# Optimization experiments

Measured on AMD Instinct MI355X. Metric: run time of the kernel, lower is better.

The kernel has to match this reference:

```python
import jax, jax.numpy as jnp
import numpy as np

EPS = 1e-8


def setup_inputs() -> dict:
    key = jax.random.key(0)
    k1, k2, k3 = jax.random.split(key, 3)
    N, M, D = 200000, 64, 128
    X = jax.random.normal(k1, (N, D), dtype=jnp.float32)
    r = jax.random.uniform(k2, (N, M), dtype=jnp.float32)
    mus = jax.random.normal(k3, (M, D), dtype=jnp.float32)
    return {"X": X, "r": r, "mus": mus}


def _pairwise_l2_sim(X, mus):
    # sim = -||x - mu||_2, computed via the Gram trick to avoid an [N,M,D] intermediate
    x2 = jnp.sum(X * X, axis=-1, keepdims=True)          # [N,1]
    m2 = jnp.sum(mus * mus, axis=-1)[None, :]            # [1,M]
    sq = x2 + m2 - 2.0 * (X @ mus.T)                     # [N,M]
    return -jnp.sqrt(jnp.maximum(sq, 0.0))


def reference(X, r, mus):
    N = X.shape[0]
    sim = _pairwise_l2_sim(X, mus)                       # [N,M]
    sim_z = -jnp.log(jax.nn.sigmoid(sim) + EPS)          # [N,M]
    loss = jnp.sum(r * sim_z) / N
    return loss
```

## Files before the change

### kernel.cpp

```cpp
#include <hip/hip_runtime.h>
#include <math.h>

#define D_DIM 128
#define M_CLUSTERS 64
#define ROWS 64
#define BLOCK 256
#define RBLOCK 256

typedef __bf16 bf16x8 __attribute__((ext_vector_type(8)));
typedef float f32x4 __attribute__((ext_vector_type(4)));

union B8 {
    int4 i;
    bf16x8 b;
};

__device__ __forceinline__ float zval(float sq) {
    float dd = sqrtf(fmaxf(sq, 0.0f));
    float sg = __fdividef(1.0f, 1.0f + __expf(dd));
    return -__logf(sg + 1e-8f);
}

__device__ __forceinline__ void gload16(const void* g, void* l) {
    __builtin_amdgcn_global_load_lds(
        (const __attribute__((address_space(1))) unsigned int*)g,
        (__attribute__((address_space(3))) unsigned int*)l, 16, 0, 0);
}

__global__ void iso_prep(const float4* __restrict__ mus4, int4* __restrict__ muB4,
                         float* __restrict__ m2) {
    const int f = blockIdx.x * 256 + threadIdx.x;
    float4 v0 = mus4[f * 2 + 0];
    float4 v1 = mus4[f * 2 + 1];
    B8 p;
    p.b[0] = (__bf16)v0.x; p.b[1] = (__bf16)v0.y;
    p.b[2] = (__bf16)v0.z; p.b[3] = (__bf16)v0.w;
    p.b[4] = (__bf16)v1.x; p.b[5] = (__bf16)v1.y;
    p.b[6] = (__bf16)v1.z; p.b[7] = (__bf16)v1.w;
    muB4[f] = p.i;
    if (blockIdx.x == 0 && threadIdx.x < M_CLUSTERS) {
        const float4* mv = mus4 + threadIdx.x * (D_DIM / 4);
        float s = 0.f;
#pragma unroll
        for (int d = 0; d < D_DIM / 4; ++d) {
            float4 v = mv[d];
            s = fmaf(v.x, v.x, s);
            s = fmaf(v.y, v.y, s);
            s = fmaf(v.z, v.z, s);
            s = fmaf(v.w, v.w, s);
        }
        m2[threadIdx.x] = s;
    }
}

__global__ __launch_bounds__(BLOCK, 4) void iso_main(
        const float* __restrict__ X, const float* __restrict__ r,
        const int4* __restrict__ muB4, const float* __restrict__ m2g,
        float* __restrict__ partials, int N) {
    __shared__ __align__(16) char lds_raw[ROWS * 512 + M_CLUSTERS * 256];
    __shared__ float pl[BLOCK];

    const int tid = threadIdx.x;
    const int lane = tid & 63;
    const int la = lane & 15;
    const int lg = lane >> 4;
    const int w = tid >> 6;
    const int rowbase = blockIdx.x * ROWS;

    char* xs = lds_raw;
    char* bs = lds_raw + ROWS * 512;

#pragma unroll
    for (int c = 0; c < 8; ++c) {
        int rr = c * 2 + (lane >> 5);
        int grow = rowbase + w * 16 + rr;
        grow = grow < N ? grow : N - 1;
        int slot = (lane & 31) ^ (rr & 7);
        gload16(X + (size_t)grow * D_DIM + slot * 4,
                xs + (size_t)w * 8192 + c * 1024);
    }
#pragma unroll
    for (int i = 0; i < 4; ++i) {
        int k = w * 4 + i;
        int c = k * 4 + (lane >> 4);
        int slot = (lane & 15) ^ (c & 7);
        gload16(muB4 + c * 16 + slot, bs + k * 1024);
    }

    float rv[4][4];
    const int erow = rowbase + w * 16 + lg * 4;
#pragma unroll
    for (int q = 0; q < 4; ++q) {
        int rrow = erow + q;
        const float* rr_ = r + (size_t)(rrow < N ? rrow : N - 1) * M_CLUSTERS + la;
#pragma unroll
        for (int cb = 0; cb < 4; ++cb)
            rv[q][cb] = (rrow < N) ? rr_[cb * 16] : 0.f;
    }
    float m2r[4];
#pragma unroll
    for (int cb = 0; cb < 4; ++cb) m2r[cb] = m2g[cb * 16 + la];

    asm volatile("s_waitcnt vmcnt(0)" ::: "memory");
    __syncthreads();

    f32x4 acc[4];
#pragma unroll
    for (int cb = 0; cb < 4; ++cb)
#pragma unroll
        for (int q = 0; q < 4; ++q) acc[cb][q] = 0.f;
    float x2 = 0.f;

    const char* xw = xs + (size_t)w * 8192;
#pragma unroll
    for (int kk = 0; kk < 4; ++kk) {
        int s0 = kk * 8 + lg * 2;
        float4 xa = *(const float4*)(xw + la * 512 + ((s0) ^ (la & 7)) * 16);
        float4 xb = *(const float4*)(xw + la * 512 + ((s0 + 1) ^ (la & 7)) * 16);
        B8 a;
        a.b[0] = (__bf16)xa.x; a.b[1] = (__bf16)xa.y;
        a.b[2] = (__bf16)xa.z; a.b[3] = (__bf16)xa.w;
        a.b[4] = (__bf16)xb.x; a.b[5] = (__bf16)xb.y;
        a.b[6] = (__bf16)xb.z; a.b[7] = (__bf16)xb.w;
        x2 = fmaf(xa.x, xa.x, x2); x2 = fmaf(xa.y, xa.y, x2);
        x2 = fmaf(xa.z, xa.z, x2); x2 = fmaf(xa.w, xa.w, x2);
        x2 = fmaf(xb.x, xb.x, x2); x2 = fmaf(xb.y, xb.y, x2);
        x2 = fmaf(xb.z, xb.z, x2); x2 = fmaf(xb.w, xb.w, x2);
        B8 b[4];
#pragma unroll
        for (int cb = 0; cb < 4; ++cb) {
            int cc = cb * 16 + la;
            int t = (kk * 4 + lg) ^ (cc & 7);
            b[cb].i = *(const int4*)(bs + cc * 256 + t * 16);
        }
#pragma unroll
        for (int cb = 0; cb < 4; ++cb)
            acc[cb] = __builtin_amdgcn_mfma_f32_16x16x32_bf16(a.b, b[cb].b,
                                                              acc[cb], 0, 0, 0);
    }

    x2 += __shfl_xor(x2, 16, 64);
    x2 += __shfl_xor(x2, 32, 64);
    float x2r[4];
#pragma unroll
    for (int q = 0; q < 4; ++q) x2r[q] = __shfl(x2, lg * 4 + q, 64);

    float partial = 0.f;
#pragma unroll
    for (int q = 0; q < 4; ++q)
#pragma unroll
        for (int cb = 0; cb < 4; ++cb) {
            float sq = x2r[q] + m2r[cb] - 2.0f * acc[cb][q];
            partial = fmaf(rv[q][cb], zval(sq), partial);
        }

    pl[tid] = partial;
    __syncthreads();
    if (tid < 64) {
        float s = pl[lane] + pl[64 + lane] + pl[128 + lane] + pl[192 + lane];
#pragma unroll
        for (int off = 32; off > 0; off >>= 1)
            s += __shfl_down(s, off, 64);
        if (lane == 0) partials[blockIdx.x] = s;
    }
}

__global__ void iso_reduce(const float* __restrict__ partials, int nblocks,
                           float* __restrict__ out, float invN) {
    float s = 0.f;
    for (int i = threadIdx.x; i < nblocks; i += RBLOCK) s += partials[i];
#pragma unroll
    for (int off = 32; off > 0; off >>= 1)
        s += __shfl_down(s, off, 64);
    __shared__ float wsum[RBLOCK / 64];
    const int lane = threadIdx.x & 63;
    const int wid = threadIdx.x >> 6;
    if (lane == 0) wsum[wid] = s;
    __syncthreads();
    if (threadIdx.x == 0)
        out[0] = (wsum[0] + wsum[1] + wsum[2] + wsum[3]) * invN;
}

extern "C" void kernel_launch(void* const* d_in, const int* in_sizes, int n_in,
                              void* d_out, int out_size, void* d_ws, size_t ws_size,
                              hipStream_t stream) {
    const float* X = (const float*)d_in[0];
    const float* r = (const float*)d_in[1];
    const float* mus = (const float*)d_in[2];
    const int N = in_sizes[0] / D_DIM;

    int4* muB4 = (int4*)d_ws;
    float* m2 = (float*)((char*)d_ws + 16384);
    float* partials = m2 + M_CLUSTERS;

    const int nblocks = (N + ROWS - 1) / ROWS;

    hipLaunchKernelGGL(iso_prep, dim3(4), dim3(256), 0, stream,
                       (const float4*)mus, muB4, m2);
    hipLaunchKernelGGL(iso_main, dim3(nblocks), dim3(BLOCK), 0, stream,
                       X, r, muB4, m2, partials, N);
    hipLaunchKernelGGL(iso_reduce, dim3(1), dim3(RBLOCK), 0, stream,
                       partials, nblocks, (float*)d_out, 1.0f / (float)N);
}
```

Before: 42.76 us.

## Process four row tiles per block and prefetch next X tile during epilogue

Each block now loops over four 64-row tiles instead of one, so the block count drops by four. The bf16 mu matrix and m2 are loaded into LDS once per block. After each tile's MFMA phase, the next tile's X rows are issued asynchronously into the same LDS buffer, so the load overlaps the sqrt/exp/log epilogue and the loads of r. The goal is to hide global-load latency and amortise setup. In exchange there is less block-level parallelism, a single X buffer, and one wasted prefetch past the last tile. The __syncthreads before the vmcnt wait may not guarantee that the mu LDS copies issued by other waves are visible.

New measurement: 48.12 us. 1.13x slower.

```diff
diff --git a/kernel.cpp b/kernel.cpp
--- a/kernel.cpp
+++ b/kernel.cpp
@@ -3,7 +3,8 @@
 
 #define D_DIM 128
 #define M_CLUSTERS 64
-#define ROWS 64
+#define TILE_ROWS 64
+#define TPB 4
 #define BLOCK 256
 #define RBLOCK 256
 
@@ -57,7 +58,8 @@
         const float* __restrict__ X, const float* __restrict__ r,
         const int4* __restrict__ muB4, const float* __restrict__ m2g,
         float* __restrict__ partials, int N) {
-    __shared__ __align__(16) char lds_raw[ROWS * 512 + M_CLUSTERS * 256];
+    __shared__ __align__(16) char xs_raw[4 * 8192];
+    __shared__ __align__(16) char bs_raw[16384];
     __shared__ float pl[BLOCK];
 
     const int tid = threadIdx.x;
@@ -65,20 +67,13 @@
     const int la = lane & 15;
     const int lg = lane >> 4;
     const int w = tid >> 6;
-    const int rowbase = blockIdx.x * ROWS;
-
-    char* xs = lds_raw;
-    char* bs = lds_raw + ROWS * 512;
-
-#pragma unroll
-    for (int c = 0; c < 8; ++c) {
-        int rr = c * 2 + (lane >> 5);
-        int grow = rowbase + w * 16 + rr;
-        grow = grow < N ? grow : N - 1;
-        int slot = (lane & 31) ^ (rr & 7);
-        gload16(X + (size_t)grow * D_DIM + slot * 4,
-                xs + (size_t)w * 8192 + c * 1024);
-    }
+
+    char* xw = xs_raw + w * 8192;
+    char* bs = bs_raw;
+
+    const int rr = (lane >> 5);
+    const int xslot = (lane & 31);
+
 #pragma unroll
     for (int i = 0; i < 4; ++i) {
         int k = w * 4 + i;
@@ -86,73 +81,104 @@
         int slot = (lane & 15) ^ (c & 7);
         gload16(muB4 + c * 16 + slot, bs + k * 1024);
     }
-
-    float rv[4][4];
-    const int erow = rowbase + w * 16 + lg * 4;
-#pragma unroll
-    for (int q = 0; q < 4; ++q) {
-        int rrow = erow + q;
-        const float* rr_ = r + (size_t)(rrow < N ? rrow : N - 1) * M_CLUSTERS + la;
+    {
+        int rowbase = blockIdx.x * (TPB * TILE_ROWS) + w * 16;
+#pragma unroll
+        for (int c = 0; c < 8; ++c) {
+            int row = c * 2 + rr;
+            int grow = rowbase + row;
+            grow = grow < N ? grow : N - 1;
+            int slot = xslot ^ (row & 7);
+            gload16(X + (size_t)grow * D_DIM + slot * 4, xw + c * 1024);
+        }
+    }
+    float m2r[4];
+#pragma unroll
+    for (int cb = 0; cb < 4; ++cb) m2r[cb] = m2g[cb * 16 + la];
+    __syncthreads();
+
+    float partial = 0.f;
+
+    for (int t = 0; t < TPB; ++t) {
+        const int rowbase = (blockIdx.x * TPB + t) * TILE_ROWS + w * 16;
+
+        float rv[4][4];
+        const int erow = rowbase + lg * 4;
+#pragma unroll
+        for (int q = 0; q < 4; ++q) {
+            int rrow = erow + q;
+            const float* rr_ =
+                r + (size_t)(rrow < N ? rrow : N - 1) * M_CLUSTERS + la;
+#pragma unroll
+            for (int cb = 0; cb < 4; ++cb)
+                rv[q][cb] = (rrow < N) ? rr_[cb * 16] : 0.f;
+        }
+
+        asm volatile("s_waitcnt vmcnt(16)" ::: "memory");
+        __builtin_amdgcn_sched_barrier(0);
+
+        f32x4 acc[4];
 #pragma unroll
         for (int cb = 0; cb < 4; ++cb)
-            rv[q][cb] = (rrow < N) ? rr_[cb * 16] : 0.f;
-    }
-    float m2r[4];
-#pragma unroll
-    for (int cb = 0; cb < 4; ++cb) m2r[cb] = m2g[cb * 16 + la];
-
-    asm volatile("s_waitcnt vmcnt(0)" ::: "memory");
-    __syncthreads();
-
-    f32x4 acc[4];
-#pragma unroll
-    for (int cb = 0; cb < 4; ++cb)
-#pragma unroll
-        for (int q = 0; q < 4; ++q) acc[cb][q] = 0.f;
-    float x2 = 0.f;
-
-    const char* xw = xs + (size_t)w * 8192;
-#pragma unroll
-    for (int kk = 0; kk < 4; ++kk) {
-        int s0 = kk * 8 + lg * 2;
-        float4 xa = *(const float4*)(xw + la * 512 + ((s0) ^ (la & 7)) * 16);
-        float4 xb = *(const float4*)(xw + la * 512 + ((s0 + 1) ^ (la & 7)) * 16);
-        B8 a;
-        a.b[0] = (__bf16)xa.x; a.b[1] = (__bf16)xa.y;
-        a.b[2] = (__bf16)xa.z; a.b[3] = (__bf16)xa.w;
-        a.b[4] = (__bf16)xb.x; a.b[5] = (__bf16)xb.y;
-        a.b[6] = (__bf16)xb.z; a.b[7] = (__bf16)xb.w;
-        x2 = fmaf(xa.x, xa.x, x2); x2 = fmaf(xa.y, xa.y, x2);
-        x2 = fmaf(xa.z, xa.z, x2); x2 = fmaf(xa.w, xa.w, x2);
-        x2 = fmaf(xb.x, xb.x, x2); x2 = fmaf(xb.y, xb.y, x2);
-        x2 = fmaf(xb.z, xb.z, x2); x2 = fmaf(xb.w, xb.w, x2);
-        B8 b[4];
-#pragma unroll
-        for (int cb = 0; cb < 4; ++cb) {
-            int cc = cb * 16 + la;
-            int t = (kk * 4 + lg) ^ (cc & 7);
-            b[cb].i = *(const int4*)(bs + cc * 256 + t * 16);
-        }
-#pragma unroll
-        for (int cb = 0; cb < 4; ++cb)
-            acc[cb] = __builtin_amdgcn_mfma_f32_16x16x32_bf16(a.b, b[cb].b,
-                                                              acc[cb], 0, 0, 0);
-    }
-
-    x2 += __shfl_xor(x2, 16, 64);
-    x2 += __shfl_xor(x2, 32, 64);
-    float x2r[4];
-#pragma unroll
-    for (int q = 0; q < 4; ++q) x2r[q] = __shfl(x2, lg * 4 + q, 64);
-
-    float partial = 0.f;
-#pragma unroll
-    for (int q = 0; q < 4; ++q)
-#pragma unroll
-        for (int cb = 0; cb < 4; ++cb) {
-            float sq = x2r[q] + m2r[cb] - 2.0f * acc[cb][q];
-            partial = fmaf(rv[q][cb], zval(sq), partial);
-        }
+#pragma unroll
+            for (int q = 0; q < 4; ++q) acc[cb][q] = 0.f;
+        float x2 = 0.f;
+
+#pragma unroll
+        for (int kk = 0; kk < 4; ++kk) {
+            int s0 = kk * 8 + lg * 2;
+            float4 xa = *(const float4*)(xw + la * 512 + ((s0) ^ (la & 7)) * 16);
+            float4 xb = *(const float4*)(xw + la * 512 + ((s0 + 1) ^ (la & 7)) * 16);
+            B8 a;
+            a.b[0] = (__bf16)xa.x; a.b[1] = (__bf16)xa.y;
+            a.b[2] = (__bf16)xa.z; a.b[3] = (__bf16)xa.w;
+            a.b[4] = (__bf16)xb.x; a.b[5] = (__bf16)xb.y;
+            a.b[6] = (__bf16)xb.z; a.b[7] = (__bf16)xb.w;
+            x2 = fmaf(xa.x, xa.x, x2); x2 = fmaf(xa.y, xa.y, x2);
+            x2 = fmaf(xa.z, xa.z, x2); x2 = fmaf(xa.w, xa.w, x2);
+            x2 = fmaf(xb.x, xb.x, x2); x2 = fmaf(xb.y, xb.y, x2);
+            x2 = fmaf(xb.z, xb.z, x2); x2 = fmaf(xb.w, xb.w, x2);
+            B8 b[4];
+#pragma unroll
+            for (int cb = 0; cb < 4; ++cb) {
+                int cc = cb * 16 + la;
+                int tt = (kk * 4 + lg) ^ (cc & 7);
+                b[cb].i = *(const int4*)(bs + cc * 256 + tt * 16);
+            }
+#pragma unroll
+            for (int cb = 0; cb < 4; ++cb)
+                acc[cb] = __builtin_amdgcn_mfma_f32_16x16x32_bf16(
+                    a.b, b[cb].b, acc[cb], 0, 0, 0);
+        }
+
+        asm volatile("s_waitcnt lgkmcnt(0)" ::: "memory");
+        __builtin_amdgcn_sched_barrier(0);
+        {
+            int nrowbase = rowbase + TILE_ROWS;
+#pragma unroll
+            for (int c = 0; c < 8; ++c) {
+                int row = c * 2 + rr;
+                int grow = nrowbase + row;
+                grow = grow < N ? grow : N - 1;
+                int slot = xslot ^ (row & 7);
+                gload16(X + (size_t)grow * D_DIM + slot * 4, xw + c * 1024);
+            }
+        }
+
+        x2 += __shfl_xor(x2, 16, 64);
+        x2 += __shfl_xor(x2, 32, 64);
+        float x2r[4];
+#pragma unroll
+        for (int q = 0; q < 4; ++q) x2r[q] = __shfl(x2, lg * 4 + q, 64);
+
+#pragma unroll
+        for (int q = 0; q < 4; ++q)
+#pragma unroll
+            for (int cb = 0; cb < 4; ++cb) {
+                float sq = x2r[q] + m2r[cb] - 2.0f * acc[cb][q];
+                partial = fmaf(rv[q][cb], zval(sq), partial);
+            }
+    }
 
     pl[tid] = partial;
     __syncthreads();
@@ -193,7 +219,8 @@
     float* m2 = (float*)((char*)d_ws + 16384);
     float* partials = m2 + M_CLUSTERS;
 
-    const int nblocks = (N + ROWS - 1) / ROWS;
+    const int ntiles = (N + TILE_ROWS - 1) / TILE_ROWS;
+    const int nblocks = (ntiles + TPB - 1) / TPB;
 
     hipLaunchKernelGGL(iso_prep, dim3(4), dim3(256), 0, stream,
                        (const float4*)mus, muB4, m2);
```

## Convert main kernel to persistent waves with double-buffered X staging

Applied to the files above, without the earlier changes.

Replaces the one-tile-per-block grid with a fixed persistent grid in which each wave loops over 16-row tiles. It double-buffers X into LDS via async global-to-LDS loads, using explicit vmcnt waits to overlap the next tile's load with the current MFMA and epilogue. The bf16 centroid fragments and m2 are held in registers for the whole kernel instead of being reloaded through LDS per block, and per-block partials shrink to the grid size. This adds hand-tuned waitcnt accounting that is fragile, and tiling assumes N is a multiple of 16 for full coverage.

After: 44.53 us. 4.2% more time.

```diff
diff --git a/kernel.cpp b/kernel.cpp
--- a/kernel.cpp
+++ b/kernel.cpp
@@ -3,8 +3,10 @@
 
 #define D_DIM 128
 #define M_CLUSTERS 64
-#define ROWS 64
-#define BLOCK 256
+#define BLOCK 512
+#define GRID 256
+#define WPB 8
+#define TOTAL_WAVES (GRID * WPB)
 #define RBLOCK 256
 
 typedef __bf16 bf16x8 __attribute__((ext_vector_type(8)));
@@ -26,6 +28,18 @@
         (const __attribute__((address_space(1))) unsigned int*)g,
         (__attribute__((address_space(3))) unsigned int*)l, 16, 0, 0);
 }
+
+#define LOADF(dst, ptr, OFF)                                        \
+    asm volatile("global_load_dword %0, %1, off offset:" #OFF       \
+                 : "=v"(dst) : "v"(ptr) : "memory")
+#define LOADX4(dst, ptr, OFF)                                       \
+    asm volatile("global_load_dwordx4 %0, %1, off offset:" #OFF     \
+                 : "=v"(dst) : "v"(ptr) : "memory")
+#define WAITVM(N_)                                                  \
+    do {                                                            \
+        asm volatile("s_waitcnt vmcnt(" #N_ ")" ::: "memory");      \
+        __builtin_amdgcn_sched_barrier(0);                          \
+    } while (0)
 
 __global__ void iso_prep(const float4* __restrict__ mus4, int4* __restrict__ muB4,
                          float* __restrict__ m2) {
@@ -53,57 +67,21 @@
     }
 }
 
-__global__ __launch_bounds__(BLOCK, 4) void iso_main(
-        const float* __restrict__ X, const float* __restrict__ r,
-        const int4* __restrict__ muB4, const float* __restrict__ m2g,
-        float* __restrict__ partials, int N) {
-    __shared__ __align__(16) char lds_raw[ROWS * 512 + M_CLUSTERS * 256];
-    __shared__ float pl[BLOCK];
-
-    const int tid = threadIdx.x;
-    const int lane = tid & 63;
-    const int la = lane & 15;
-    const int lg = lane >> 4;
-    const int w = tid >> 6;
-    const int rowbase = blockIdx.x * ROWS;
-
-    char* xs = lds_raw;
-    char* bs = lds_raw + ROWS * 512;
-
-#pragma unroll
-    for (int c = 0; c < 8; ++c) {
-        int rr = c * 2 + (lane >> 5);
-        int grow = rowbase + w * 16 + rr;
-        grow = grow < N ? grow : N - 1;
-        int slot = (lane & 31) ^ (rr & 7);
-        gload16(X + (size_t)grow * D_DIM + slot * 4,
-                xs + (size_t)w * 8192 + c * 1024);
-    }
-#pragma unroll
-    for (int i = 0; i < 4; ++i) {
-        int k = w * 4 + i;
-        int c = k * 4 + (lane >> 4);
-        int slot = (lane & 15) ^ (c & 7);
-        gload16(muB4 + c * 16 + slot, bs + k * 1024);
-    }
-
-    float rv[4][4];
-    const int erow = rowbase + w * 16 + lg * 4;
-#pragma unroll
-    for (int q = 0; q < 4; ++q) {
-        int rrow = erow + q;
-        const float* rr_ = r + (size_t)(rrow < N ? rrow : N - 1) * M_CLUSTERS + la;
-#pragma unroll
-        for (int cb = 0; cb < 4; ++cb)
-            rv[q][cb] = (rrow < N) ? rr_[cb * 16] : 0.f;
-    }
-    float m2r[4];
-#pragma unroll
-    for (int cb = 0; cb < 4; ++cb) m2r[cb] = m2g[cb * 16 + la];
-
-    asm volatile("s_waitcnt vmcnt(0)" ::: "memory");
-    __syncthreads();
-
+__device__ __forceinline__ void load_rv(const float* rp, float (&rv)[4][4]) {
+    LOADF(rv[0][0], rp, 0);   LOADF(rv[0][1], rp, 64);
+    LOADF(rv[0][2], rp, 128); LOADF(rv[0][3], rp, 192);
+    LOADF(rv[1][0], rp, 256); LOADF(rv[1][1], rp, 320);
+    LOADF(rv[1][2], rp, 384); LOADF(rv[1][3], rp, 448);
+    LOADF(rv[2][0], rp, 512); LOADF(rv[2][1], rp, 576);
+    LOADF(rv[2][2], rp, 640); LOADF(rv[2][3], rp, 704);
+    LOADF(rv[3][0], rp, 768); LOADF(rv[3][1], rp, 832);
+    LOADF(rv[3][2], rp, 896); LOADF(rv[3][3], rp, 960);
+}
+
+template <int VMEPI>
+__device__ __forceinline__ float compute_tile(
+        const char* cur, int la, int lg,
+        const B8 (&bfr)[4][4], const float (&m2r)[4], const float (&rv)[4][4]) {
     f32x4 acc[4];
 #pragma unroll
     for (int cb = 0; cb < 4; ++cb)
@@ -111,12 +89,13 @@
         for (int q = 0; q < 4; ++q) acc[cb][q] = 0.f;
     float x2 = 0.f;
 
-    const char* xw = xs + (size_t)w * 8192;
+    const char* xrow = cur + la * 512;
+    const int sw = la & 7;
 #pragma unroll
     for (int kk = 0; kk < 4; ++kk) {
         int s0 = kk * 8 + lg * 2;
-        float4 xa = *(const float4*)(xw + la * 512 + ((s0) ^ (la & 7)) * 16);
-        float4 xb = *(const float4*)(xw + la * 512 + ((s0 + 1) ^ (la & 7)) * 16);
+        float4 xa = *(const float4*)(xrow + ((s0) ^ sw) * 16);
+        float4 xb = *(const float4*)(xrow + ((s0 + 1) ^ sw) * 16);
         B8 a;
         a.b[0] = (__bf16)xa.x; a.b[1] = (__bf16)xa.y;
         a.b[2] = (__bf16)xa.z; a.b[3] = (__bf16)xa.w;
@@ -126,17 +105,10 @@
         x2 = fmaf(xa.z, xa.z, x2); x2 = fmaf(xa.w, xa.w, x2);
         x2 = fmaf(xb.x, xb.x, x2); x2 = fmaf(xb.y, xb.y, x2);
         x2 = fmaf(xb.z, xb.z, x2); x2 = fmaf(xb.w, xb.w, x2);
-        B8 b[4];
-#pragma unroll
-        for (int cb = 0; cb < 4; ++cb) {
-            int cc = cb * 16 + la;
-            int t = (kk * 4 + lg) ^ (cc & 7);
-            b[cb].i = *(const int4*)(bs + cc * 256 + t * 16);
-        }
 #pragma unroll
         for (int cb = 0; cb < 4; ++cb)
-            acc[cb] = __builtin_amdgcn_mfma_f32_16x16x32_bf16(a.b, b[cb].b,
-                                                              acc[cb], 0, 0, 0);
+            acc[cb] = __builtin_amdgcn_mfma_f32_16x16x32_bf16(
+                a.b, bfr[cb][kk].b, acc[cb], 0, 0, 0);
     }
 
     x2 += __shfl_xor(x2, 16, 64);
@@ -145,23 +117,114 @@
 #pragma unroll
     for (int q = 0; q < 4; ++q) x2r[q] = __shfl(x2, lg * 4 + q, 64);
 
-    float partial = 0.f;
+    if constexpr (VMEPI == 8) { WAITVM(8); } else { WAITVM(0); }
+
+    float p = 0.f;
 #pragma unroll
     for (int q = 0; q < 4; ++q)
 #pragma unroll
         for (int cb = 0; cb < 4; ++cb) {
             float sq = x2r[q] + m2r[cb] - 2.0f * acc[cb][q];
-            partial = fmaf(rv[q][cb], zval(sq), partial);
+            p = fmaf(rv[q][cb], zval(sq), p);
         }
+    return p;
+}
+
+__global__ __launch_bounds__(BLOCK, 2) void iso_main(
+        const float* __restrict__ X, const float* __restrict__ r,
+        const int4* __restrict__ muB4, const float* __restrict__ m2g,
+        float* __restrict__ partials, int N) {
+    __shared__ __align__(16) char xs[WPB * 2 * 8192];
+    __shared__ float pl[BLOCK];
+
+    const int tid = threadIdx.x;
+    const int lane = tid & 63;
+    const int la = lane & 15;
+    const int lg = lane >> 4;
+    const int w = tid >> 6;
+    const int gid = blockIdx.x * WPB + w;
+
+    char* xb0 = xs + w * 16384;
+    char* xb1 = xb0 + 8192;
+
+    const int ntiles = N >> 4;
+    const int full = ntiles / TOTAL_WAVES;
+    const int rem = ntiles - full * TOTAL_WAVES;
+
+    const int srow = lane >> 5;
+    const int sslot = lane & 31;
+
+    auto stage = [&](int t, char* dst) {
+        int tt = t < ntiles ? t : ntiles - 1;
+#pragma unroll
+        for (int c = 0; c < 8; ++c) {
+            int row = c * 2 + srow;
+            int grow = tt * 16 + row;
+            grow = grow < N ? grow : N - 1;
+            int slot = sslot ^ (row & 7);
+            gload16(X + (size_t)grow * D_DIM + slot * 4, dst + c * 1024);
+        }
+    };
+
+    float m2r[4];
+    {
+        const float* mp = m2g + la;
+        LOADF(m2r[0], mp, 0);
+        LOADF(m2r[1], mp, 64);
+        LOADF(m2r[2], mp, 128);
+        LOADF(m2r[3], mp, 192);
+    }
+    B8 bfr[4][4];
+    {
+        const int4* bp = muB4 + la * 16 + lg;
+        LOADX4(bfr[0][0].i, bp, 0);  LOADX4(bfr[0][1].i, bp, 64);
+        LOADX4(bfr[0][2].i, bp, 128); LOADX4(bfr[0][3].i, bp, 192);
+        const int4* bp1 = bp + 256;
+        LOADX4(bfr[1][0].i, bp1, 0);  LOADX4(bfr[1][1].i, bp1, 64);
+        LOADX4(bfr[1][2].i, bp1, 128); LOADX4(bfr[1][3].i, bp1, 192);
+        const int4* bp2 = bp + 512;
+        LOADX4(bfr[2][0].i, bp2, 0);  LOADX4(bfr[2][1].i, bp2, 64);
+        LOADX4(bfr[2][2].i, bp2, 128); LOADX4(bfr[2][3].i, bp2, 192);
+        const int4* bp3 = bp + 768;
+        LOADX4(bfr[3][0].i, bp3, 0);  LOADX4(bfr[3][1].i, bp3, 64);
+        LOADX4(bfr[3][2].i, bp3, 128); LOADX4(bfr[3][3].i, bp3, 192);
+    }
+    stage(gid, xb0);
+    __builtin_amdgcn_sched_barrier(0);
+
+    float partial = 0.f;
+
+    for (int k = 0; k < full; ++k) {
+        const int tk = k * TOTAL_WAVES + gid;
+        float rv[4][4];
+        const float* rp = r + ((size_t)tk * 16 + lg * 4) * M_CLUSTERS + la;
+        load_rv(rp, rv);
+        stage(tk + TOTAL_WAVES, (k & 1) ? xb0 : xb1);
+        WAITVM(24);
+        const char* cur = (k & 1) ? xb1 : xb0;
+        partial += compute_tile<8>(cur, la, lg, bfr, m2r, rv);
+    }
+
+    if (gid < rem) {
+        const int tk = full * TOTAL_WAVES + gid;
+        float rv[4][4];
+        const float* rp = r + ((size_t)tk * 16 + lg * 4) * M_CLUSTERS + la;
+        load_rv(rp, rv);
+        WAITVM(16);
+        const char* cur = (full & 1) ? xb1 : xb0;
+        partial += compute_tile<0>(cur, la, lg, bfr, m2r, rv);
+    }
 
     pl[tid] = partial;
     __syncthreads();
     if (tid < 64) {
-        float s = pl[lane] + pl[64 + lane] + pl[128 + lane] + pl[192 + lane];
+        float s = 0.f;
+#pragma unroll
+        for (int j = 0; j < WPB; ++j) s += pl[j * 64 + tid];
 #pragma unroll
         for (int off = 32; off > 0; off >>= 1)
             s += __shfl_down(s, off, 64);
-        if (lane == 0) partials[blockIdx.x] = s;
+        if (tid == 0) partials[blockIdx.x] = s;
     }
 }
 
@@ -193,12 +256,10 @@
     float* m2 = (float*)((char*)d_ws + 16384);
     float* partials = m2 + M_CLUSTERS;
 
-    const int nblocks = (N + ROWS - 1) / ROWS;
-
     hipLaunchKernelGGL(iso_prep, dim3(4), dim3(256), 0, stream,
                        (const float4*)mus, muB4, m2);
-    hipLaunchKernelGGL(iso_main, dim3(nblocks), dim3(BLOCK), 0, stream,
+    hipLaunchKernelGGL(iso_main, dim3(GRID), dim3(BLOCK), 0, stream,
                        X, r, muB4, m2, partials, N);
     hipLaunchKernelGGL(iso_reduce, dim3(1), dim3(RBLOCK), 0, stream,
-                       partials, nblocks, (float*)d_out, 1.0f / (float)N);
-}
+                       partials, GRID, (float*)d_out, 1.0f / (float)N);
+}
```
